# Kernel tuning notes

Measured on AMD Instinct MI355X. Metric: run time of the kernel, lower is better.

## Reference

```python
import jax, jax.numpy as jnp
import numpy as np

D_MODEL = 1024
NUM_HEADS = 16
D_K = D_MODEL // NUM_HEADS


def setup_inputs() -> dict:
    key = jax.random.key(0)
    ks = jax.random.split(key, 11)
    B, S = 2, 2048
    scale = 1.0 / np.sqrt(D_MODEL)
    inp = {
        'Q': jax.random.normal(ks[0], (B, S, D_MODEL), dtype=jnp.float32),
        'K': jax.random.normal(ks[1], (B, S, D_MODEL), dtype=jnp.float32),
        'V': jax.random.normal(ks[2], (B, S, D_MODEL), dtype=jnp.float32),
        'Wq': jax.random.normal(ks[3], (D_MODEL, D_MODEL), dtype=jnp.float32) * scale,
        'bq': jax.random.normal(ks[4], (D_MODEL,), dtype=jnp.float32) * scale,
        'Wk': jax.random.normal(ks[5], (D_MODEL, D_MODEL), dtype=jnp.float32) * scale,
        'bk': jax.random.normal(ks[6], (D_MODEL,), dtype=jnp.float32) * scale,
        'Wv': jax.random.normal(ks[7], (D_MODEL, D_MODEL), dtype=jnp.float32) * scale,
        'bv': jax.random.normal(ks[8], (D_MODEL,), dtype=jnp.float32) * scale,
        'Wo': jax.random.normal(ks[9], (D_MODEL, D_MODEL), dtype=jnp.float32) * scale,
        'bo': jax.random.normal(ks[10], (D_MODEL,), dtype=jnp.float32) * scale,
    }
    return inp


def _split_heads(x):
    B, S, _ = x.shape
    return x.reshape(B, S, NUM_HEADS, D_K).transpose(0, 2, 1, 3)  # [B,H,S,dk]


def reference(Q, K, V, Wq, bq, Wk, bk, Wv, bv, Wo, bo):
    # Linear projections (torch Linear: x @ W.T + b)
    q = _split_heads(Q @ Wq.T + bq)
    k = _split_heads(K @ Wk.T + bk)
    v = _split_heads(V @ Wv.T + bv)
    scores = jnp.einsum('bhqd,bhkd->bhqk', q, k) / jnp.sqrt(jnp.float32(D_K))
    probs = jax.nn.softmax(scores, axis=-1)
    out = jnp.einsum('bhqk,bhkd->bhqd', probs, v)  # [B,H,S,dk]
    B, H, S, dk = out.shape
    out = out.transpose(0, 2, 1, 3).reshape(B, S, D_MODEL)
    return out @ Wo.T + bo
```

## Files before the change

kernel.cpp:

```cpp
#include <hip/hip_runtime.h>
#include <hip/hip_bf16.h>

#define DEV __device__ __forceinline__

#define BATCH 2
#define SEQ   2048
#define DMODEL 1024
#define NHEAD 16
#define DK    64
#define MROWS (BATCH*SEQ)
#define KD    1024
#define GEMM_NT (KD/32)
#define ATTN_NT (SEQ/64)

#define QSCALE 0.18033688011112042f

typedef __attribute__((ext_vector_type(4))) float f32x4;
typedef __attribute__((ext_vector_type(8))) short s16x8;
typedef __attribute__((ext_vector_type(4))) short s16x4;
typedef __attribute__((ext_vector_type(4))) float fvec4;
typedef __attribute__((ext_vector_type(2))) unsigned int u32x2;
typedef __attribute__((ext_vector_type(4))) unsigned int u32x4;

__device__ short g_X[3][MROWS*DMODEL];
__device__ short g_W[4][DMODEL*DMODEL];
__device__ short g_q [MROWS*DMODEL];
__device__ short g_k [MROWS*DMODEL];
__device__ short g_vt[MROWS*DMODEL];
__device__ short g_at[MROWS*DMODEL];

DEV short f2bf(float f) {
  union { __hip_bfloat16 h; short s; } u;
  u.h = __float2bfloat16(f);
  return u.s;
}

DEV unsigned int f2bf2(float lo, float hi) {
  unsigned int r;
  asm("v_cvt_pk_bf16_f32 %0, %1, %2" : "=v"(r) : "v"(lo), "v"(hi));
  return r;
}

DEV void gload_lds16(const void* g, void* l) {
  __builtin_amdgcn_global_load_lds(
      (const __attribute__((address_space(1))) void*)g,
      (__attribute__((address_space(3))) void*)l, 16, 0, 0);
}

__global__ __launch_bounds__(256) void cast3(const float* __restrict__ a,
                                             const float* __restrict__ b,
                                             const float* __restrict__ c, int n8) {
  const float* src = blockIdx.z == 0 ? a : blockIdx.z == 1 ? b : c;
  short* dst = g_X[blockIdx.z];
  int i = blockIdx.x * 256 + threadIdx.x;
  if (i < n8) {
    const fvec4* p = (const fvec4*)(src + (size_t)i*8);
    fvec4 v0 = p[0], v1 = p[1];
    u32x4 r;
    r[0] = f2bf2(v0[0], v0[1]); r[1] = f2bf2(v0[2], v0[3]);
    r[2] = f2bf2(v1[0], v1[1]); r[3] = f2bf2(v1[2], v1[3]);
    *(u32x4*)(dst + (size_t)i*8) = r;
  }
}

__global__ __launch_bounds__(256) void cast4(const float* __restrict__ a,
                                             const float* __restrict__ b,
                                             const float* __restrict__ c,
                                             const float* __restrict__ d, int n8) {
  const float* src = blockIdx.z == 0 ? a : blockIdx.z == 1 ? b
                   : blockIdx.z == 2 ? c : d;
  short* dst = g_W[blockIdx.z];
  int i = blockIdx.x * 256 + threadIdx.x;
  if (i < n8) {
    const fvec4* p = (const fvec4*)(src + (size_t)i*8);
    fvec4 v0 = p[0], v1 = p[1];
    u32x4 r;
    r[0] = f2bf2(v0[0], v0[1]); r[1] = f2bf2(v0[2], v0[3]);
    r[2] = f2bf2(v1[0], v1[1]); r[3] = f2bf2(v1[2], v1[3]);
    *(u32x4*)(dst + (size_t)i*8) = r;
  }
}

struct GemmSmem { short As[3][128*32]; short Bs[3][128*32]; };

DEV void gemm_core(GemmSmem& sm, const short* __restrict__ A,
                   const short* __restrict__ Bw, const float* __restrict__ bias,
                   void* __restrict__ outp, float scale, int mode,
                   int rowBase, int colBase) {
  const int t = threadIdx.x, l = t & 63, w = t >> 6, g = l >> 4;
  const int wr = w >> 1, wc = w & 1;

  f32x4 acc[4][4] = {};

  auto stage = [&](int buf, int k0) {
#pragma unroll
    for (int j = 0; j < 2; ++j) {
      int e = w*1024 + j*512 + l*8;
      int e2 = e ^ (((e >> 7) & 3) << 3);
      int r = e2 >> 5, c = e2 & 31;
      gload_lds16(A  + (size_t)(rowBase + r)*KD + k0 + c, &sm.As[buf][w*1024 + j*512]);
      gload_lds16(Bw + (size_t)(colBase + r)*KD + k0 + c, &sm.Bs[buf][w*1024 + j*512]);
    }
  };

  stage(0, 0);
  stage(1, 32);

  int cur = 0, nxt = 2;
  for (int i = 0; i < GEMM_NT; ++i) {
    if (i < GEMM_NT - 1) asm volatile("s_waitcnt vmcnt(4)" ::: "memory");
    else                 asm volatile("s_waitcnt vmcnt(0)" ::: "memory");
    __builtin_amdgcn_s_barrier();
    __builtin_amdgcn_sched_barrier(0);

    s16x8 a[4], b[4];
#pragma unroll
    for (int x = 0; x < 4; ++x) {
      int ra = wr*64 + x*16 + (l & 15);
      int ia = (ra*32 + g*8) ^ (((ra >> 2) & 3) << 3);
      a[x] = *(const s16x8*)&sm.As[cur][ia];
      int rb = wc*64 + x*16 + (l & 15);
      int ib = (rb*32 + g*8) ^ (((rb >> 2) & 3) << 3);
      b[x] = *(const s16x8*)&sm.Bs[cur][ib];
    }
    if (i + 2 < GEMM_NT) stage(nxt, (i + 2)*32);
    __builtin_amdgcn_sched_barrier(0);

    __builtin_amdgcn_s_setprio(1);
#pragma unroll
    for (int x = 0; x < 4; ++x)
#pragma unroll
      for (int jn = 0; jn < 4; ++jn)
        acc[x][jn] = __builtin_amdgcn_mfma_f32_16x16x32_bf16(a[x], b[jn], acc[x][jn], 0, 0, 0);
    __builtin_amdgcn_s_setprio(0);

    cur = cur == 2 ? 0 : cur + 1;
    nxt = nxt == 2 ? 0 : nxt + 1;
  }

#pragma unroll
  for (int x = 0; x < 4; ++x) {
    int mrow0 = rowBase + wr*64 + x*16 + g*4;
#pragma unroll
    for (int jn = 0; jn < 4; ++jn) {
      int n = colBase + wc*64 + jn*16 + (l & 15);
      float bv = bias[n];
      float val[4];
#pragma unroll
      for (int r = 0; r < 4; ++r) val[r] = (acc[x][jn][r] + bv) * scale;
      if (mode == 3) {
#pragma unroll
        for (int r = 0; r < 4; ++r)
          ((float*)outp)[(size_t)(mrow0 + r)*DMODEL + n] = val[r];
      } else {
        unsigned int pk0 = f2bf2(val[0], val[1]);
        unsigned int pk1 = f2bf2(val[2], val[3]);
        int h = n >> 6, d = n & 63;
#pragma unroll
        for (int r = 0; r < 4; ++r) {
          int m = mrow0 + r;
          int b = m >> 11, s = m & 2047;
          unsigned int pk = r < 2 ? pk0 : pk1;
          short sv = (short)((r & 1) ? (pk >> 16) : (pk & 0xffff));
          if (mode == 1)
            ((short*)outp)[(((size_t)(b*NHEAD + h)*SEQ + s)*DK) + d] = sv;
          else
            ((short*)outp)[((size_t)(b*NHEAD + h)*DK + d)*SEQ + s] = sv;
        }
      }
    }
  }
}

__global__ __launch_bounds__(256, 3)
void proj_qkv(const float* __restrict__ bq, const float* __restrict__ bk,
              const float* __restrict__ bv) {
  __shared__ GemmSmem sm;
  int z = blockIdx.z;
  int orig = blockIdx.y*8 + blockIdx.x;
  int swz = (orig & 7)*32 + (orig >> 3);
  int bx = swz & 7, by = swz >> 3;
  const float* bias = z == 0 ? bq : z == 1 ? bk : bv;
  void* outp = z == 0 ? (void*)g_q : z == 1 ? (void*)g_k : (void*)g_vt;
  gemm_core(sm, g_X[z], g_W[z], bias, outp, z == 0 ? QSCALE : 1.0f,
            z == 2 ? 2 : 1, by*128, bx*128);
}

__global__ __launch_bounds__(256, 3)
void proj_out(const float* __restrict__ bo, float* __restrict__ out) {
  __shared__ GemmSmem sm;
  int orig = blockIdx.y*8 + blockIdx.x;
  int swz = (orig & 7)*32 + (orig >> 3);
  int bx = swz & 7, by = swz >> 3;
  gemm_core(sm, g_at, g_W[3], bo, out, 1.0f, 3, by*128, bx*128);
}

__global__ __launch_bounds__(512, 4)
void attn_kernel(short* __restrict__ aout) {
  __shared__ short ps[128*64];
  __shared__ short ks[3][64*64];
  __shared__ short vs[3][64*64];

  const int t = threadIdx.x, l = t & 63, w = t >> 6, g = l >> 4;
  const int q15 = l & 15;
  int orig = blockIdx.y*16 + blockIdx.x;
  int swz = (orig & 7)*64 + (orig >> 3);
  const int qblk = swz & 15, bh = swz >> 4;
  const int qbase = qblk * 128;
  const size_t hoff = (size_t)bh * SEQ * DK;

  auto stage_kv = [&](int buf, int kt) {
    int e = t*8;
    int e2 = e ^ (((e >> 6) & 7) << 3);
    gload_lds16(g_k + hoff + (size_t)kt*DK + e2, &ks[buf][e]);
    gload_lds16(g_vt + hoff + (size_t)(e2 >> 6)*SEQ + kt + (e2 & 63), &vs[buf][e]);
  };

  s16x8 qf[2];
  {
    const short* qrow = g_q + hoff + (size_t)(qbase + w*16 + q15)*DK;
    qf[0] = *(const s16x8*)(qrow + g*8);
    qf[1] = *(const s16x8*)(qrow + 32 + g*8);
  }
  stage_kv(0, 0);
  stage_kv(1, 64);

  float lsum = 0.f;
  f32x4 o[4] = {};

  int cur = 0, nxt = 2;
  for (int i = 0; i < ATTN_NT; ++i) {
    if (i < ATTN_NT - 1) asm volatile("s_waitcnt vmcnt(2)" ::: "memory");
    else                 asm volatile("s_waitcnt vmcnt(0)" ::: "memory");
    __builtin_amdgcn_s_barrier();
    __builtin_amdgcn_sched_barrier(0);

    s16x8 kfr[4][2];
#pragma unroll
    for (int ni = 0; ni < 4; ++ni)
#pragma unroll
      for (int kf = 0; kf < 2; ++kf) {
        int row = ni*16 + q15;
        int idx = (row*64 + kf*32 + g*8) ^ ((row & 7) << 3);
        kfr[ni][kf] = *(const s16x8*)&ks[cur][idx];
      }
    if (i + 2 < ATTN_NT) stage_kv(nxt, (i + 2)*64);
    __builtin_amdgcn_sched_barrier(0);

    f32x4 sc[4] = {};
    __builtin_amdgcn_s_setprio(1);
#pragma unroll
    for (int ni = 0; ni < 4; ++ni)
#pragma unroll
      for (int kf = 0; kf < 2; ++kf)
        sc[ni] = __builtin_amdgcn_mfma_f32_16x16x32_bf16(kfr[ni][kf], qf[kf], sc[ni], 0, 0, 0);
    __builtin_amdgcn_s_setprio(0);

    float p[4][4];
#pragma unroll
    for (int ni = 0; ni < 4; ++ni)
#pragma unroll
      for (int r = 0; r < 4; ++r)
        p[ni][r] = exp2f(sc[ni][r]);

    float s0 = (p[0][0]+p[0][1]) + (p[0][2]+p[0][3]);
    float s1 = (p[1][0]+p[1][1]) + (p[1][2]+p[1][3]);
    float s2 = (p[2][0]+p[2][1]) + (p[2][2]+p[2][3]);
    float s3 = (p[3][0]+p[3][1]) + (p[3][2]+p[3][3]);
    lsum += (s0+s1) + (s2+s3);

#pragma unroll
    for (int ni = 0; ni < 4; ++ni) {
      u32x2 pv;
      pv[0] = f2bf2(p[ni][0], p[ni][1]);
      pv[1] = f2bf2(p[ni][2], p[ni][3]);
      int idx = w*1024 + q15*64 + ((ni*16 + g*4) ^ ((q15 & 7) << 3));
      *(u32x2*)&ps[idx] = pv;
    }

    asm volatile("s_waitcnt lgkmcnt(0)" ::: "memory");
    __builtin_amdgcn_sched_barrier(0);

    s16x8 pa[2];
#pragma unroll
    for (int kf = 0; kf < 2; ++kf) {
      int idx = w*1024 + q15*64 + ((kf*32 + g*8) ^ ((q15 & 7) << 3));
      pa[kf] = *(const s16x8*)&ps[idx];
    }

    __builtin_amdgcn_s_setprio(1);
#pragma unroll
    for (int nd = 0; nd < 4; ++nd)
#pragma unroll
      for (int kf = 0; kf < 2; ++kf) {
        int row = nd*16 + q15;
        int idx = (row*64 + kf*32 + g*8) ^ ((row & 7) << 3);
        s16x8 bfr = *(const s16x8*)&vs[cur][idx];
        o[nd] = __builtin_amdgcn_mfma_f32_16x16x32_bf16(pa[kf], bfr, o[nd], 0, 0, 0);
      }
    __builtin_amdgcn_s_setprio(0);

    cur = cur == 2 ? 0 : cur + 1;
    nxt = nxt == 2 ? 0 : nxt + 1;
  }

  lsum += __shfl_xor(lsum, 16);
  lsum += __shfl_xor(lsum, 32);
  float inv = 1.0f / lsum;
  float iv[4];
#pragma unroll
  for (int r = 0; r < 4; ++r)
    iv[r] = __shfl(inv, (l & 48) | (g*4 + r));

  int b = bh >> 4, h = bh & 15;
#pragma unroll
  for (int nd = 0; nd < 4; ++nd) {
    int dcol = h*DK + nd*16 + q15;
#pragma unroll
    for (int r = 0; r < 4; ++r) {
      int srow = qbase + w*16 + g*4 + r;
      aout[((size_t)(b*SEQ + srow))*DMODEL + dcol] = f2bf(o[nd][r] * iv[r]);
    }
  }
}

extern "C" void kernel_launch(void* const* d_in, const int* in_sizes, int n_in,
                              void* d_out, int out_size, void* d_ws, size_t ws_size,
                              hipStream_t stream) {
  const float* Q  = (const float*)d_in[0];
  const float* K  = (const float*)d_in[1];
  const float* V  = (const float*)d_in[2];
  const float* Wq = (const float*)d_in[3];
  const float* bq = (const float*)d_in[4];
  const float* Wk = (const float*)d_in[5];
  const float* bk = (const float*)d_in[6];
  const float* Wv = (const float*)d_in[7];
  const float* bv = (const float*)d_in[8];
  const float* Wo = (const float*)d_in[9];
  const float* bo = (const float*)d_in[10];

  short* pat;
  hipGetSymbolAddress((void**)&pat, HIP_SYMBOL(g_at));

  const int nX8 = MROWS*DMODEL/8;
  const int nW8 = DMODEL*DMODEL/8;
  dim3 blk(256);

  cast3<<<dim3(nX8/256, 1, 3), blk, 0, stream>>>(Q, K, V, nX8);
  cast4<<<dim3(nW8/256, 1, 4), blk, 0, stream>>>(Wq, Wk, Wv, Wo, nW8);
  proj_qkv<<<dim3(DMODEL/128, MROWS/128, 3), blk, 0, stream>>>(bq, bk, bv);
  attn_kernel<<<dim3(SEQ/128, BATCH*NHEAD), dim3(512), 0, stream>>>(pat);
  proj_out<<<dim3(DMODEL/128, MROWS/128), blk, 0, stream>>>(bo, (float*)d_out);
}
```

Measured before the change: 145.6 us.

## Split attention KV tiles across wave pairs, register-shuffle P, and merge partials

The attention kernel now gives each wave 32 query rows instead of 16. The eight waves split into two groups that handle alternate 64-key tiles from a four-slot pair-staged K/V buffer, so each K/V fragment read from LDS feeds twice as many MFMAs. The probability tile is rearranged into MFMA operand layout with permlane swaps instead of a round trip through LDS. The two key-halves' partial outputs and row sums are then merged through shared memory at the end. This removes the LDS writes and reads for P and halves K/V fragment loads per output. The cost is more registers per wave, a full vmcnt(0) wait before every pair of tiles, and an extra reduction epilogue.

```diff
diff --git a/kernel.cpp b/kernel.cpp
--- a/kernel.cpp
+++ b/kernel.cpp
@@ -11,13 +11,11 @@
 #define MROWS (BATCH*SEQ)
 #define KD    1024
 #define GEMM_NT (KD/32)
-#define ATTN_NT (SEQ/64)
 
 #define QSCALE 0.18033688011112042f
 
 typedef __attribute__((ext_vector_type(4))) float f32x4;
 typedef __attribute__((ext_vector_type(8))) short s16x8;
-typedef __attribute__((ext_vector_type(4))) short s16x4;
 typedef __attribute__((ext_vector_type(4))) float fvec4;
 typedef __attribute__((ext_vector_type(2))) unsigned int u32x2;
 typedef __attribute__((ext_vector_type(4))) unsigned int u32x4;
@@ -45,6 +43,10 @@
   __builtin_amdgcn_global_load_lds(
       (const __attribute__((address_space(1))) void*)g,
       (__attribute__((address_space(3))) void*)l, 16, 0, 0);
+}
+
+DEV f32x4 mfma16(s16x8 a, s16x8 b, f32x4 c) {
+  return __builtin_amdgcn_mfma_f32_16x16x32_bf16(a, b, c, 0, 0, 0);
 }
 
 __global__ __launch_bounds__(256) void cast3(const float* __restrict__ a,
@@ -131,7 +133,7 @@
     for (int x = 0; x < 4; ++x)
 #pragma unroll
       for (int jn = 0; jn < 4; ++jn)
-        acc[x][jn] = __builtin_amdgcn_mfma_f32_16x16x32_bf16(a[x], b[jn], acc[x][jn], 0, 0, 0);
+        acc[x][jn] = mfma16(a[x], b[jn], acc[x][jn]);
     __builtin_amdgcn_s_setprio(0);
 
     cur = cur == 2 ? 0 : cur + 1;
@@ -197,129 +199,159 @@
 
 __global__ __launch_bounds__(512, 4)
 void attn_kernel(short* __restrict__ aout) {
-  __shared__ short ps[128*64];
-  __shared__ short ks[3][64*64];
-  __shared__ short vs[3][64*64];
+  __shared__ short ks[4][64*64];
+  __shared__ short vs[4][64*64];
 
   const int t = threadIdx.x, l = t & 63, w = t >> 6, g = l >> 4;
   const int q15 = l & 15;
+  const int qg = w & 3, kp = w >> 2;
   int orig = blockIdx.y*16 + blockIdx.x;
   int swz = (orig & 7)*64 + (orig >> 3);
   const int qblk = swz & 15, bh = swz >> 4;
   const int qbase = qblk * 128;
   const size_t hoff = (size_t)bh * SEQ * DK;
 
-  auto stage_kv = [&](int buf, int kt) {
+  auto stage_pair = [&](int pr) {
     int e = t*8;
     int e2 = e ^ (((e >> 6) & 7) << 3);
-    gload_lds16(g_k + hoff + (size_t)kt*DK + e2, &ks[buf][e]);
-    gload_lds16(g_vt + hoff + (size_t)(e2 >> 6)*SEQ + kt + (e2 & 63), &vs[buf][e]);
+    int t0 = 2*pr, t1 = t0 + 1;
+    gload_lds16(g_k + hoff + (size_t)(t0*64)*DK + e2, &ks[t0 & 3][e]);
+    gload_lds16(g_k + hoff + (size_t)(t1*64)*DK + e2, &ks[t1 & 3][e]);
+    gload_lds16(g_vt + hoff + (size_t)(e2 >> 6)*SEQ + t0*64 + (e2 & 63), &vs[t0 & 3][e]);
+    gload_lds16(g_vt + hoff + (size_t)(e2 >> 6)*SEQ + t1*64 + (e2 & 63), &vs[t1 & 3][e]);
   };
 
-  s16x8 qf[2];
+  s16x8 qf[2][2];
   {
-    const short* qrow = g_q + hoff + (size_t)(qbase + w*16 + q15)*DK;
-    qf[0] = *(const s16x8*)(qrow + g*8);
-    qf[1] = *(const s16x8*)(qrow + 32 + g*8);
-  }
-  stage_kv(0, 0);
-  stage_kv(1, 64);
-
-  float lsum = 0.f;
-  f32x4 o[4] = {};
-
-  int cur = 0, nxt = 2;
-  for (int i = 0; i < ATTN_NT; ++i) {
-    if (i < ATTN_NT - 1) asm volatile("s_waitcnt vmcnt(2)" ::: "memory");
-    else                 asm volatile("s_waitcnt vmcnt(0)" ::: "memory");
+    const short* q0 = g_q + hoff + (size_t)(qbase + qg*32 + q15)*DK;
+    qf[0][0] = *(const s16x8*)(q0 + g*8);
+    qf[0][1] = *(const s16x8*)(q0 + 32 + g*8);
+    qf[1][0] = *(const s16x8*)(q0 + 16*DK + g*8);
+    qf[1][1] = *(const s16x8*)(q0 + 16*DK + 32 + g*8);
+  }
+  stage_pair(0);
+
+  float lsum[2] = {0.f, 0.f};
+  f32x4 o[2][4] = {};
+
+  for (int i = 0; i < 16; ++i) {
+    asm volatile("s_waitcnt vmcnt(0)" ::: "memory");
     __builtin_amdgcn_s_barrier();
     __builtin_amdgcn_sched_barrier(0);
-
-    s16x8 kfr[4][2];
-#pragma unroll
-    for (int ni = 0; ni < 4; ++ni)
+    if (i + 1 < 16) stage_pair(i + 1);
+
+    const short* kb = ks[(2*i + kp) & 3];
+    const short* vb = vs[(2*i + kp) & 3];
+
+    f32x4 sc[2][4] = {};
+    __builtin_amdgcn_s_setprio(1);
+#pragma unroll
+    for (int ni = 0; ni < 4; ++ni) {
+      int row = ni*16 + q15;
+      int sx = (row & 7) << 3;
+      s16x8 k0 = *(const s16x8*)&kb[(row*64 + g*8) ^ sx];
+      s16x8 k1 = *(const s16x8*)&kb[(row*64 + 32 + g*8) ^ sx];
+      sc[0][ni] = mfma16(k0, qf[0][0], sc[0][ni]);
+      sc[0][ni] = mfma16(k1, qf[0][1], sc[0][ni]);
+      sc[1][ni] = mfma16(k0, qf[1][0], sc[1][ni]);
+      sc[1][ni] = mfma16(k1, qf[1][1], sc[1][ni]);
+    }
+    __builtin_amdgcn_s_setprio(0);
+
+    s16x8 pa[2][2];
+#pragma unroll
+    for (int grp = 0; grp < 2; ++grp) {
+      float p[4][4];
+#pragma unroll
+      for (int ni = 0; ni < 4; ++ni)
+#pragma unroll
+        for (int r = 0; r < 4; ++r)
+          p[ni][r] = exp2f(sc[grp][ni][r]);
+      float s0 = (p[0][0]+p[0][1]) + (p[0][2]+p[0][3]);
+      float s1 = (p[1][0]+p[1][1]) + (p[1][2]+p[1][3]);
+      float s2 = (p[2][0]+p[2][1]) + (p[2][2]+p[2][3]);
+      float s3 = (p[3][0]+p[3][1]) + (p[3][2]+p[3][3]);
+      lsum[grp] += (s0+s1) + (s2+s3);
+
+      unsigned pk[4][2];
+#pragma unroll
+      for (int ni = 0; ni < 4; ++ni) {
+        pk[ni][0] = f2bf2(p[ni][0], p[ni][1]);
+        pk[ni][1] = f2bf2(p[ni][2], p[ni][3]);
+      }
 #pragma unroll
       for (int kf = 0; kf < 2; ++kf) {
-        int row = ni*16 + q15;
-        int idx = (row*64 + kf*32 + g*8) ^ ((row & 7) << 3);
-        kfr[ni][kf] = *(const s16x8*)&ks[cur][idx];
+        u32x4 P4;
+#pragma unroll
+        for (int u = 0; u < 2; ++u) {
+          unsigned x = pk[2*kf][u], y = pk[2*kf + 1][u];
+          asm("v_permlane32_swap_b32 %0, %1" : "+v"(x), "+v"(y));
+          asm("v_permlane16_swap_b32 %0, %1" : "+v"(x), "+v"(y));
+          P4[u]     = x;
+          P4[2 + u] = y;
+        }
+        union { u32x4 u4; s16x8 s8; } cv;
+        cv.u4 = P4;
+        pa[grp][kf] = cv.s8;
       }
-    if (i + 2 < ATTN_NT) stage_kv(nxt, (i + 2)*64);
-    __builtin_amdgcn_sched_barrier(0);
-
-    f32x4 sc[4] = {};
+    }
+
     __builtin_amdgcn_s_setprio(1);
 #pragma unroll
-    for (int ni = 0; ni < 4; ++ni)
-#pragma unroll
-      for (int kf = 0; kf < 2; ++kf)
-        sc[ni] = __builtin_amdgcn_mfma_f32_16x16x32_bf16(kfr[ni][kf], qf[kf], sc[ni], 0, 0, 0);
+    for (int nd = 0; nd < 4; ++nd) {
+      int row = nd*16 + q15;
+      int sx = (row & 7) << 3;
+      s16x8 v0 = *(const s16x8*)&vb[(row*64 + g*8) ^ sx];
+      s16x8 v1 = *(const s16x8*)&vb[(row*64 + 32 + g*8) ^ sx];
+      o[0][nd] = mfma16(pa[0][0], v0, o[0][nd]);
+      o[0][nd] = mfma16(pa[0][1], v1, o[0][nd]);
+      o[1][nd] = mfma16(pa[1][0], v0, o[1][nd]);
+      o[1][nd] = mfma16(pa[1][1], v1, o[1][nd]);
+    }
     __builtin_amdgcn_s_setprio(0);
-
-    float p[4][4];
-#pragma unroll
-    for (int ni = 0; ni < 4; ++ni)
+  }
+
+  __syncthreads();
+  float* ob = (float*)&vs[0][0];
+  float* lb = (float*)&ks[0][0];
+  if (kp) {
+#pragma unroll
+    for (int grp = 0; grp < 2; ++grp) {
+#pragma unroll
+      for (int nd = 0; nd < 4; ++nd)
+#pragma unroll
+        for (int r = 0; r < 4; ++r)
+          ob[(qg*32 + grp*16 + nd*4 + r)*64 + l] = o[grp][nd][r];
+      lb[(qg*2 + grp)*64 + l] = lsum[grp];
+    }
+  }
+  __syncthreads();
+  if (!kp) {
+    int b = bh >> 4, h = bh & 15;
+#pragma unroll
+    for (int grp = 0; grp < 2; ++grp) {
+#pragma unroll
+      for (int nd = 0; nd < 4; ++nd)
+#pragma unroll
+        for (int r = 0; r < 4; ++r)
+          o[grp][nd][r] += ob[(qg*32 + grp*16 + nd*4 + r)*64 + l];
+      float ls = lsum[grp] + lb[(qg*2 + grp)*64 + l];
+      ls += __shfl_xor(ls, 16);
+      ls += __shfl_xor(ls, 32);
+      float inv = 1.0f / ls;
+      float iv[4];
 #pragma unroll
       for (int r = 0; r < 4; ++r)
-        p[ni][r] = exp2f(sc[ni][r]);
-
-    float s0 = (p[0][0]+p[0][1]) + (p[0][2]+p[0][3]);
-    float s1 = (p[1][0]+p[1][1]) + (p[1][2]+p[1][3]);
-    float s2 = (p[2][0]+p[2][1]) + (p[2][2]+p[2][3]);
-    float s3 = (p[3][0]+p[3][1]) + (p[3][2]+p[3][3]);
-    lsum += (s0+s1) + (s2+s3);
-
-#pragma unroll
-    for (int ni = 0; ni < 4; ++ni) {
-      u32x2 pv;
-      pv[0] = f2bf2(p[ni][0], p[ni][1]);
-      pv[1] = f2bf2(p[ni][2], p[ni][3]);
-      int idx = w*1024 + q15*64 + ((ni*16 + g*4) ^ ((q15 & 7) << 3));
-      *(u32x2*)&ps[idx] = pv;
-    }
-
-    asm volatile("s_waitcnt lgkmcnt(0)" ::: "memory");
-    __builtin_amdgcn_sched_barrier(0);
-
-    s16x8 pa[2];
-#pragma unroll
-    for (int kf = 0; kf < 2; ++kf) {
-      int idx = w*1024 + q15*64 + ((kf*32 + g*8) ^ ((q15 & 7) << 3));
-      pa[kf] = *(const s16x8*)&ps[idx];
-    }
-
-    __builtin_amdgcn_s_setprio(1);
-#pragma unroll
-    for (int nd = 0; nd < 4; ++nd)
-#pragma unroll
-      for (int kf = 0; kf < 2; ++kf) {
-        int row = nd*16 + q15;
-        int idx = (row*64 + kf*32 + g*8) ^ ((row & 7) << 3);
-        s16x8 bfr = *(const s16x8*)&vs[cur][idx];
-        o[nd] = __builtin_amdgcn_mfma_f32_16x16x32_bf16(pa[kf], bfr, o[nd], 0, 0, 0);
+        iv[r] = __shfl(inv, (l & 48) | (g*4 + r));
+#pragma unroll
+      for (int nd = 0; nd < 4; ++nd) {
+        int dcol = h*DK + nd*16 + q15;
+#pragma unroll
+        for (int r = 0; r < 4; ++r) {
+          int srow = qbase + qg*32 + grp*16 + g*4 + r;
+          aout[((size_t)(b*SEQ + srow))*DMODEL + dcol] = f2bf(o[grp][nd][r] * iv[r]);
+        }
       }
-    __builtin_amdgcn_s_setprio(0);
-
-    cur = cur == 2 ? 0 : cur + 1;
-    nxt = nxt == 2 ? 0 : nxt + 1;
-  }
-
-  lsum += __shfl_xor(lsum, 16);
-  lsum += __shfl_xor(lsum, 32);
-  float inv = 1.0f / lsum;
-  float iv[4];
-#pragma unroll
-  for (int r = 0; r < 4; ++r)
-    iv[r] = __shfl(inv, (l & 48) | (g*4 + r));
-
-  int b = bh >> 4, h = bh & 15;
-#pragma unroll
-  for (int nd = 0; nd < 4; ++nd) {
-    int dcol = h*DK + nd*16 + q15;
-#pragma unroll
-    for (int r = 0; r < 4; ++r) {
-      int srow = qbase + w*16 + g*4 + r;
-      aout[((size_t)(b*SEQ + srow))*DMODEL + dcol] = f2bf(o[nd][r] * iv[r]);
     }
   }
 }
```

New measurement: 149.6 us. 2.8% more time.
